# Kernel tuning notes

Measured on AMD Instinct MI355X. Metric: run time of the kernel, lower is better.

Reference implementation:

```python
import jax, jax.numpy as jnp
import numpy as np

TOPK = 2


def setup_inputs() -> dict:
    key = jax.random.key(0)
    k1, k2, k3, k4, k5 = jax.random.split(key, 5)
    D, H, E = 1024, 1408, 8
    hidden_states = jax.random.normal(k1, (2, 1024, D), dtype=jnp.float32)
    gate_w = jax.random.normal(k2, (E, D), dtype=jnp.float32) * 0.02
    w1g = jax.random.normal(k3, (E, D, H), dtype=jnp.float32) * 0.02
    w1u = jax.random.normal(k4, (E, D, H), dtype=jnp.float32) * 0.02
    w2 = jax.random.normal(k5, (E, H, D), dtype=jnp.float32) * 0.02
    return {"hidden_states": hidden_states, "gate_w": gate_w, "w1g": w1g, "w1u": w1u, "w2": w2}


def reference(hidden_states, gate_w, w1g, w1u, w2):
    # hidden_states: [B, S, D]; expert weights: w1g/w1u [E, D, H], w2 [E, H, D]
    B, S, D = hidden_states.shape
    E = gate_w.shape[0]
    x = hidden_states.reshape(-1, D)  # [T, D]
    T = x.shape[0]

    # --- MoEGate: softmax scores, top-k routing (no topk renorm) ---
    logits = x @ gate_w.T                      # [T, E]
    scores = jax.nn.softmax(logits, axis=-1)   # [T, E]
    topk_w, topk_idx = jax.lax.top_k(scores, TOPK)  # [T, K]

    # Per-token combine coefficient for each expert: coeff[t, e] = sum_k w[t,k] * (idx[t,k]==e)
    coeff = jnp.zeros((T, E), dtype=x.dtype).at[jnp.arange(T)[:, None], topk_idx].add(topk_w)

    # --- Grouped expert MLP (swiglu): identical math to permute + grouped GEMM + unpermute ---
    g = jnp.einsum('td,edh->teh', x, w1g)      # [T, E, H]
    u = jnp.einsum('td,edh->teh', x, w1u)      # [T, E, H]
    h = jax.nn.silu(g) * u                     # [T, E, H]
    y = jnp.einsum('teh,te,ehd->td', h, coeff, w2)  # [T, D]
    return y.reshape(B, S, D)
```

## Files before the change

### kernel.cpp

```cpp
#include <hip/hip_runtime.h>

#define TOK 2048
#define DDIM 1024
#define HDIM 1408
#define ENUM 8
#define NSLOT (2 * TOK)
#define UP_NB 22
#define UP_KS 32
#define DN_NB 16
#define DN_KS 44

typedef unsigned int uint;
typedef unsigned short ushort;

using bf16x8 = __attribute__((ext_vector_type(8))) __bf16;
using f32x4  = __attribute__((ext_vector_type(4))) float;

__device__ __forceinline__ float silu_f(float g) {
    return g / (1.0f + __expf(-g));
}

__device__ __forceinline__ ushort cvt_bf16(float f) {
    uint u = __float_as_uint(f);
    u += 0x7FFFu + ((u >> 16) & 1u);
    return (ushort)(u >> 16);
}

__device__ __forceinline__ void gl2lds16(const void* g, void* l) {
    __builtin_amdgcn_global_load_lds(
        (const __attribute__((address_space(1))) uint*)g,
        (__attribute__((address_space(3))) uint*)l, 16, 0, 0);
}

__global__ __launch_bounds__(64) void gate1_kernel(
    const float* __restrict__ x, const float* __restrict__ gw,
    int* __restrict__ tinfo, float* __restrict__ wslot, ushort* __restrict__ xb)
{
    const int t = blockIdx.x;
    const int lane = threadIdx.x;
    const float* xr = x + (size_t)t * DDIM;
    ushort* xbr = xb + (size_t)t * DDIM;
    float xv[16];
#pragma unroll
    for (int i = 0; i < 16; ++i) xv[i] = xr[lane + 64 * i];
#pragma unroll
    for (int i = 0; i < 16; ++i) xbr[lane + 64 * i] = cvt_bf16(xv[i]);
    float logit[ENUM];
#pragma unroll
    for (int e = 0; e < ENUM; ++e) {
        const float* gr = gw + (size_t)e * DDIM;
        float acc = 0.f;
#pragma unroll
        for (int i = 0; i < 16; ++i) acc += xv[i] * gr[lane + 64 * i];
#pragma unroll
        for (int s = 32; s > 0; s >>= 1) acc += __shfl_xor(acc, s, 64);
        logit[e] = acc;
    }
    if (lane == 0) {
        float mx = logit[0];
#pragma unroll
        for (int e = 1; e < ENUM; ++e) mx = fmaxf(mx, logit[e]);
        float p[ENUM]; float se = 0.f;
#pragma unroll
        for (int e = 0; e < ENUM; ++e) { p[e] = __expf(logit[e] - mx); se += p[e]; }
        float inv = 1.0f / se;
#pragma unroll
        for (int e = 0; e < ENUM; ++e) p[e] *= inv;
        int i0 = 0;
#pragma unroll
        for (int e = 1; e < ENUM; ++e) if (p[e] > p[i0]) i0 = e;
        int i1 = (i0 == 0) ? 1 : 0;
#pragma unroll
        for (int e = 0; e < ENUM; ++e) if (e != i0 && p[e] > p[i1]) i1 = e;
        tinfo[t] = i0 | (i1 << 4);
        wslot[(t << 1)] = p[i0];
        wslot[(t << 1) | 1] = p[i1];
    }
}

__global__ __launch_bounds__(256) void gate2_kernel(
    const int* __restrict__ tinfo, int* __restrict__ counts, int* __restrict__ toks)
{
    __shared__ int cnt[ENUM];
    const int tid = threadIdx.x;
    if (tid < ENUM) cnt[tid] = 0;
    __syncthreads();
    for (int t = tid; t < TOK; t += 256) {
        int info = tinfo[t];
        int i0 = info & 15, i1 = info >> 4;
        int p0 = atomicAdd(&cnt[i0], 1);
        toks[i0 * TOK + p0] = (t << 1);
        int p1 = atomicAdd(&cnt[i1], 1);
        toks[i1 * TOK + p1] = (t << 1) | 1;
    }
    __syncthreads();
    if (tid < ENUM) counts[tid] = cnt[tid];
}

__device__ __forceinline__ void tcast64_body(
    const float* __restrict__ src, ushort* __restrict__ dst, int N, int KS, int NB,
    int e, int ks, int nb, int tid)
{
    __shared__ float Ls[32][68];
    const float* st = src + (size_t)e * ((size_t)KS * 32) * N + (size_t)(ks * 32) * N + nb * 64;
    const int n4 = (tid & 15) * 4;
#pragma unroll
    for (int r = 0; r < 2; ++r) {
        int k = (tid >> 4) + r * 16;
        float4 v = *(const float4*)(st + (size_t)k * N + n4);
        Ls[k][n4 + 0] = v.x; Ls[k][n4 + 1] = v.y; Ls[k][n4 + 2] = v.z; Ls[k][n4 + 3] = v.w;
    }
    __syncthreads();

    ushort* dt = dst + ((((size_t)e * NB + nb) * KS) + ks) * 2048;
    const int nn = tid >> 2;
    const int kk0 = (tid & 3) * 8;
    ushort o[8];
#pragma unroll
    for (int j = 0; j < 8; ++j) o[j] = cvt_bf16(Ls[kk0 + j][nn]);
    *(uint4*)(dt + nn * 32 + kk0) = *(uint4*)o;
}

__global__ __launch_bounds__(256) void tcast_w1_kernel(
    const float* __restrict__ w1g, const float* __restrict__ w1u,
    ushort* __restrict__ BgP, ushort* __restrict__ BuP)
{
    const int z = blockIdx.z;
    const float* src = (z & 8) ? w1u : w1g;
    ushort* dst = (z & 8) ? BuP : BgP;
    tcast64_body(src, dst, HDIM, UP_KS, UP_NB, z & 7, blockIdx.x, blockIdx.y, threadIdx.x);
}

__global__ __launch_bounds__(256) void tcast_w2_kernel(
    const float* __restrict__ w2, ushort* __restrict__ W2P)
{
    tcast64_body(w2, W2P, DDIM, DN_KS, DN_NB, blockIdx.z, blockIdx.x, blockIdx.y, threadIdx.x);
}

__global__ __launch_bounds__(256, 4) void up_mfma(
    const ushort* __restrict__ xb, const ushort* __restrict__ BgP,
    const ushort* __restrict__ BuP, const int* __restrict__ counts,
    const int* __restrict__ toks, ushort* __restrict__ Hbuf)
{
    const int e = blockIdx.z;
    const int cnt = counts[e];
    const int m0 = blockIdx.y * 128;
    if (m0 >= cnt) return;
    const int nb = blockIdx.x;
    const int tid = threadIdx.x;
    const int w = tid >> 6;
    const int lane = tid & 63;
    const int q = lane >> 4;
    const int l15 = lane & 15;
    const int wr = w >> 1;
    const int wc = w & 1;

    __shared__ ushort As[2][128][32];
    __shared__ ushort Bgs[2][64][32];
    __shared__ ushort Bus[2][64][32];
    __shared__ int rowslot[128];

    if (tid < 128) rowslot[tid] = (m0 + tid < cnt) ? toks[e * TOK + m0 + tid] : -1;
    __syncthreads();

    const int srow = w * 16 + (lane >> 2);
    const int clog = (((lane & 3) + 4 - ((srow >> 1) & 3)) & 3) * 8;
    const int as0 = rowslot[srow];
    const int as1 = rowslot[srow + 64];
    const ushort* agp0 = xb + (size_t)(as0 < 0 ? 0 : (as0 >> 1)) * DDIM + clog;
    const ushort* agp1 = xb + (size_t)(as1 < 0 ? 0 : (as1 >> 1)) * DDIM + clog;
    const size_t tb = (size_t)(e * UP_NB + nb) * UP_KS * 2048;
    const ushort* bgp = BgP + tb + srow * 32 + clog;
    const ushort* bup = BuP + tb + srow * 32 + clog;

    const int coff = ((q + (l15 >> 1)) & 3) * 8;

    f32x4 accg[4][2], accu[4][2];
#pragma unroll
    for (int i = 0; i < 4; ++i)
#pragma unroll
        for (int j = 0; j < 2; ++j) { accg[i][j] = (f32x4)0.f; accu[i][j] = (f32x4)0.f; }

#define UP_PREFETCH(KSV, B)                                        \
    {                                                              \
        gl2lds16(agp0 + (KSV) * 32, &As[B][w * 16][0]);            \
        gl2lds16(agp1 + (KSV) * 32, &As[B][64 + w * 16][0]);       \
        gl2lds16(bgp + (size_t)(KSV) * 2048, &Bgs[B][w * 16][0]);  \
        gl2lds16(bup + (size_t)(KSV) * 2048, &Bus[B][w * 16][0]);  \
    }

    UP_PREFETCH(0, 0);
    __syncthreads();

    for (int ks = 0; ks < UP_KS; ++ks) {
        const int cur = ks & 1;
        const int nxt = cur ^ 1;
        if (ks + 1 < UP_KS) UP_PREFETCH(ks + 1, nxt);

        bf16x8 a[4], bg[2], bu[2];
#pragma unroll
        for (int mi = 0; mi < 4; ++mi)
            a[mi] = *(const bf16x8*)&As[cur][wr * 64 + mi * 16 + l15][coff];
#pragma unroll
        for (int ni = 0; ni < 2; ++ni) {
            bg[ni] = *(const bf16x8*)&Bgs[cur][wc * 32 + ni * 16 + l15][coff];
            bu[ni] = *(const bf16x8*)&Bus[cur][wc * 32 + ni * 16 + l15][coff];
        }
#pragma unroll
        for (int mi = 0; mi < 4; ++mi)
#pragma unroll
            for (int ni = 0; ni < 2; ++ni) {
                accg[mi][ni] = __builtin_amdgcn_mfma_f32_16x16x32_bf16(a[mi], bg[ni], accg[mi][ni], 0, 0, 0);
                accu[mi][ni] = __builtin_amdgcn_mfma_f32_16x16x32_bf16(a[mi], bu[ni], accu[mi][ni], 0, 0, 0);
            }
        __syncthreads();
    }
#undef UP_PREFETCH

#pragma unroll
    for (int mi = 0; mi < 4; ++mi) {
#pragma unroll
        for (int r = 0; r < 4; ++r) {
            int ml = wr * 64 + mi * 16 + q * 4 + r;
            int slot = rowslot[ml];
            if (slot < 0) continue;
            ushort* hrow = Hbuf + (size_t)slot * HDIM + nb * 64 + wc * 32 + l15;
#pragma unroll
            for (int ni = 0; ni < 2; ++ni)
                hrow[ni * 16] = cvt_bf16(silu_f(accg[mi][ni][r]) * accu[mi][ni][r]);
        }
    }
}

__global__ __launch_bounds__(256, 4) void down_mfma(
    const ushort* __restrict__ Hbuf, const ushort* __restrict__ W2P,
    const int* __restrict__ counts, const int* __restrict__ toks,
    float* __restrict__ Ybuf)
{
    const int e = blockIdx.z;
    const int cnt = counts[e];
    const int m0 = blockIdx.y * 128;
    if (m0 >= cnt) return;
    const int nb = blockIdx.x;
    const int tid = threadIdx.x;
    const int w = tid >> 6;
    const int lane = tid & 63;
    const int q = lane >> 4;
    const int l15 = lane & 15;
    const int wr = w >> 1;
    const int wc = w & 1;

    __shared__ ushort As[2][128][32];
    __shared__ ushort Bs[2][128][32];
    __shared__ int rowslot[128];

    if (tid < 128) rowslot[tid] = (m0 + tid < cnt) ? toks[e * TOK + m0 + tid] : -1;
    __syncthreads();

    const int srow = w * 16 + (lane >> 2);
    const int clog = (((lane & 3) + 4 - ((srow >> 1) & 3)) & 3) * 8;
    const int as0 = rowslot[srow];
    const int as1 = rowslot[srow + 64];
    const ushort* agp0 = Hbuf + (size_t)(as0 < 0 ? 0 : as0) * HDIM + clog;
    const ushort* agp1 = Hbuf + (size_t)(as1 < 0 ? 0 : as1) * HDIM + clog;
    const int nb2 = nb * 2;
    const ushort* bp0 = W2P + (size_t)(e * DN_NB + nb2) * DN_KS * 2048 + srow * 32 + clog;
    const ushort* bp1 = W2P + (size_t)(e * DN_NB + nb2 + 1) * DN_KS * 2048 + srow * 32 + clog;

    const int coff = ((q + (l15 >> 1)) & 3) * 8;

    f32x4 acc[4][4];
#pragma unroll
    for (int i = 0; i < 4; ++i)
#pragma unroll
        for (int j = 0; j < 4; ++j) acc[i][j] = (f32x4)0.f;

#define DN_PREFETCH(KSV, B)                                       \
    {                                                             \
        gl2lds16(agp0 + (KSV) * 32, &As[B][w * 16][0]);           \
        gl2lds16(agp1 + (KSV) * 32, &As[B][64 + w * 16][0]);      \
        gl2lds16(bp0 + (size_t)(KSV) * 2048, &Bs[B][w * 16][0]);  \
        gl2lds16(bp1 + (size_t)(KSV) * 2048, &Bs[B][64 + w * 16][0]); \
    }

    DN_PREFETCH(0, 0);
    __syncthreads();

    for (int ks = 0; ks < DN_KS; ++ks) {
        const int cur = ks & 1;
        const int nxt = cur ^ 1;
        if (ks + 1 < DN_KS) DN_PREFETCH(ks + 1, nxt);

        bf16x8 a[4], b[4];
#pragma unroll
        for (int mi = 0; mi < 4; ++mi)
            a[mi] = *(const bf16x8*)&As[cur][wr * 64 + mi * 16 + l15][coff];
#pragma unroll
        for (int ni = 0; ni < 4; ++ni)
            b[ni] = *(const bf16x8*)&Bs[cur][wc * 64 + ni * 16 + l15][coff];
#pragma unroll
        for (int mi = 0; mi < 4; ++mi)
#pragma unroll
            for (int ni = 0; ni < 4; ++ni)
                acc[mi][ni] = __builtin_amdgcn_mfma_f32_16x16x32_bf16(a[mi], b[ni], acc[mi][ni], 0, 0, 0);
        __syncthreads();
    }
#undef DN_PREFETCH

#pragma unroll
    for (int mi = 0; mi < 4; ++mi) {
#pragma unroll
        for (int r = 0; r < 4; ++r) {
            int ml = wr * 64 + mi * 16 + q * 4 + r;
            int slot = rowslot[ml];
            if (slot < 0) continue;
            float* yr = Ybuf + (size_t)slot * DDIM + nb * 128 + wc * 64 + l15;
#pragma unroll
            for (int ni = 0; ni < 4; ++ni)
                yr[ni * 16] = acc[mi][ni][r];
        }
    }
}

__global__ __launch_bounds__(256) void combine_kernel(
    const float* __restrict__ Ybuf, const float* __restrict__ wslot,
    float* __restrict__ y)
{
    const int t = blockIdx.x;
    const int j = threadIdx.x * 4;
    const float w0 = wslot[2 * t];
    const float w1 = wslot[2 * t + 1];
    float4 a = *(const float4*)(Ybuf + ((size_t)2 * t) * DDIM + j);
    float4 b = *(const float4*)(Ybuf + ((size_t)2 * t + 1) * DDIM + j);
    float4 o;
    o.x = w0 * a.x + w1 * b.x;
    o.y = w0 * a.y + w1 * b.y;
    o.z = w0 * a.z + w1 * b.z;
    o.w = w0 * a.w + w1 * b.w;
    *(float4*)(y + (size_t)t * DDIM + j) = o;
}

extern "C" void kernel_launch(void* const* d_in, const int* in_sizes, int n_in,
                              void* d_out, int out_size, void* d_ws, size_t ws_size,
                              hipStream_t stream) {
    const float* x   = (const float*)d_in[0];
    const float* gw  = (const float*)d_in[1];
    const float* w1g = (const float*)d_in[2];
    const float* w1u = (const float*)d_in[3];
    const float* w2  = (const float*)d_in[4];
    float* y = (float*)d_out;
    char* ws = (char*)d_ws;

    size_t off = 0;
    int*    counts = (int*)(ws + off);   off += 256;
    int*    toks   = (int*)(ws + off);   off += (size_t)ENUM * TOK * 4;
    float*  wslot  = (float*)(ws + off); off += (size_t)NSLOT * 4;
    int*    tinfo  = (int*)(ws + off);   off += (size_t)TOK * 4;
    off = (off + 255) & ~(size_t)255;
    ushort* xb     = (ushort*)(ws + off); off += (size_t)TOK * DDIM * 2;
    size_t regA = off;
    ushort* BgP  = (ushort*)(ws + regA);
    ushort* BuP  = (ushort*)(ws + regA + (size_t)ENUM * DDIM * HDIM * 2);
    float*  Ybuf = (float*)(ws + regA);
    off = regA + (size_t)2 * ENUM * DDIM * HDIM * 2;
    ushort* W2P  = (ushort*)(ws + off);  off += (size_t)ENUM * HDIM * DDIM * 2;
    ushort* Hbuf = (ushort*)(ws + off);

    gate1_kernel<<<TOK, 64, 0, stream>>>(x, gw, tinfo, wslot, xb);
    gate2_kernel<<<1, 256, 0, stream>>>(tinfo, counts, toks);

    tcast_w1_kernel<<<dim3(UP_KS, UP_NB, 16), 256, 0, stream>>>(w1g, w1u, BgP, BuP);
    tcast_w2_kernel<<<dim3(DN_KS, DN_NB, ENUM), 256, 0, stream>>>(w2, W2P);

    up_mfma<<<dim3(UP_NB, TOK / 128, ENUM), 256, 0, stream>>>(xb, BgP, BuP, counts, toks, Hbuf);
    down_mfma<<<dim3(DDIM / 128, TOK / 128, ENUM), 256, 0, stream>>>(Hbuf, W2P, counts, toks, Ybuf);
    combine_kernel<<<TOK, 256, 0, stream>>>(Ybuf, wslot, y);
}
```

Baseline: 273.5 us.

## Split down GEMM over K, fuse routing into gate, merge weight casts

The down-projection is split into two K halves, launched as extra z blocks. Each half writes a separate fp32 partial buffer, and the combine kernel sums the two. Routing is also done inside the gate kernel with global atomics after a memset, which removes the single-block gate2 kernel. The two weight-cast kernels are merged into one launch. This adds parallelism to the down GEMM and cuts launch overhead, at the cost of twice the Ybuf traffic, a larger workspace for Ybuf, and nondeterministic token order within each expert.

```diff
diff --git a/kernel.cpp b/kernel.cpp
--- a/kernel.cpp
+++ b/kernel.cpp
@@ -9,6 +9,7 @@
 #define UP_KS 32
 #define DN_NB 16
 #define DN_KS 44
+#define DN_KH 22
 
 typedef unsigned int uint;
 typedef unsigned short ushort;
@@ -34,7 +35,8 @@
 
 __global__ __launch_bounds__(64) void gate1_kernel(
     const float* __restrict__ x, const float* __restrict__ gw,
-    int* __restrict__ tinfo, float* __restrict__ wslot, ushort* __restrict__ xb)
+    int* __restrict__ counts, int* __restrict__ toks,
+    float* __restrict__ wslot, ushort* __restrict__ xb)
 {
     const int t = blockIdx.x;
     const int lane = threadIdx.x;
@@ -72,29 +74,13 @@
         int i1 = (i0 == 0) ? 1 : 0;
 #pragma unroll
         for (int e = 0; e < ENUM; ++e) if (e != i0 && p[e] > p[i1]) i1 = e;
-        tinfo[t] = i0 | (i1 << 4);
         wslot[(t << 1)] = p[i0];
         wslot[(t << 1) | 1] = p[i1];
-    }
-}
-
-__global__ __launch_bounds__(256) void gate2_kernel(
-    const int* __restrict__ tinfo, int* __restrict__ counts, int* __restrict__ toks)
-{
-    __shared__ int cnt[ENUM];
-    const int tid = threadIdx.x;
-    if (tid < ENUM) cnt[tid] = 0;
-    __syncthreads();
-    for (int t = tid; t < TOK; t += 256) {
-        int info = tinfo[t];
-        int i0 = info & 15, i1 = info >> 4;
-        int p0 = atomicAdd(&cnt[i0], 1);
+        int p0 = atomicAdd(&counts[i0], 1);
         toks[i0 * TOK + p0] = (t << 1);
-        int p1 = atomicAdd(&cnt[i1], 1);
+        int p1 = atomicAdd(&counts[i1], 1);
         toks[i1 * TOK + p1] = (t << 1) | 1;
     }
-    __syncthreads();
-    if (tid < ENUM) counts[tid] = cnt[tid];
 }
 
 __device__ __forceinline__ void tcast64_body(
@@ -121,20 +107,28 @@
     *(uint4*)(dt + nn * 32 + kk0) = *(uint4*)o;
 }
 
-__global__ __launch_bounds__(256) void tcast_w1_kernel(
+__global__ __launch_bounds__(256) void tcast_all_kernel(
     const float* __restrict__ w1g, const float* __restrict__ w1u,
-    ushort* __restrict__ BgP, ushort* __restrict__ BuP)
-{
-    const int z = blockIdx.z;
-    const float* src = (z & 8) ? w1u : w1g;
-    ushort* dst = (z & 8) ? BuP : BgP;
-    tcast64_body(src, dst, HDIM, UP_KS, UP_NB, z & 7, blockIdx.x, blockIdx.y, threadIdx.x);
-}
-
-__global__ __launch_bounds__(256) void tcast_w2_kernel(
-    const float* __restrict__ w2, ushort* __restrict__ W2P)
-{
-    tcast64_body(w2, W2P, DDIM, DN_KS, DN_NB, blockIdx.z, blockIdx.x, blockIdx.y, threadIdx.x);
+    const float* __restrict__ w2, ushort* __restrict__ BgP,
+    ushort* __restrict__ BuP, ushort* __restrict__ W2P)
+{
+    const int bid = blockIdx.x;
+    const int tid = threadIdx.x;
+    if (bid < 16 * 704) {
+        const int z = bid / 704;
+        const int rem = bid - z * 704;
+        const int nb = rem / UP_KS;
+        const int ks = rem - nb * UP_KS;
+        tcast64_body((z & 8) ? w1u : w1g, (z & 8) ? BuP : BgP,
+                     HDIM, UP_KS, UP_NB, z & 7, ks, nb, tid);
+    } else {
+        const int b2 = bid - 16 * 704;
+        const int e = b2 / 704;
+        const int rem = b2 - e * 704;
+        const int nb = rem / DN_KS;
+        const int ks = rem - nb * DN_KS;
+        tcast64_body(w2, W2P, DDIM, DN_KS, DN_NB, e, ks, nb, tid);
+    }
 }
 
 __global__ __launch_bounds__(256, 4) void up_mfma(
@@ -237,7 +231,9 @@
     const int* __restrict__ counts, const int* __restrict__ toks,
     float* __restrict__ Ybuf)
 {
-    const int e = blockIdx.z;
+    const int z = blockIdx.z;
+    const int e = z >> 1;
+    const int kh = z & 1;
     const int cnt = counts[e];
     const int m0 = blockIdx.y * 128;
     if (m0 >= cnt) return;
@@ -261,11 +257,11 @@
     const int clog = (((lane & 3) + 4 - ((srow >> 1) & 3)) & 3) * 8;
     const int as0 = rowslot[srow];
     const int as1 = rowslot[srow + 64];
-    const ushort* agp0 = Hbuf + (size_t)(as0 < 0 ? 0 : as0) * HDIM + clog;
-    const ushort* agp1 = Hbuf + (size_t)(as1 < 0 ? 0 : as1) * HDIM + clog;
+    const ushort* agp0 = Hbuf + (size_t)(as0 < 0 ? 0 : as0) * HDIM + kh * (DN_KH * 32) + clog;
+    const ushort* agp1 = Hbuf + (size_t)(as1 < 0 ? 0 : as1) * HDIM + kh * (DN_KH * 32) + clog;
     const int nb2 = nb * 2;
-    const ushort* bp0 = W2P + (size_t)(e * DN_NB + nb2) * DN_KS * 2048 + srow * 32 + clog;
-    const ushort* bp1 = W2P + (size_t)(e * DN_NB + nb2 + 1) * DN_KS * 2048 + srow * 32 + clog;
+    const ushort* bp0 = W2P + ((size_t)(e * DN_NB + nb2) * DN_KS + kh * DN_KH) * 2048 + srow * 32 + clog;
+    const ushort* bp1 = W2P + ((size_t)(e * DN_NB + nb2 + 1) * DN_KS + kh * DN_KH) * 2048 + srow * 32 + clog;
 
     const int coff = ((q + (l15 >> 1)) & 3) * 8;
 
@@ -275,21 +271,21 @@
 #pragma unroll
         for (int j = 0; j < 4; ++j) acc[i][j] = (f32x4)0.f;
 
-#define DN_PREFETCH(KSV, B)                                       \
-    {                                                             \
-        gl2lds16(agp0 + (KSV) * 32, &As[B][w * 16][0]);           \
-        gl2lds16(agp1 + (KSV) * 32, &As[B][64 + w * 16][0]);      \
-        gl2lds16(bp0 + (size_t)(KSV) * 2048, &Bs[B][w * 16][0]);  \
+#define DN_PREFETCH(KSV, B)                                           \
+    {                                                                 \
+        gl2lds16(agp0 + (KSV) * 32, &As[B][w * 16][0]);               \
+        gl2lds16(agp1 + (KSV) * 32, &As[B][64 + w * 16][0]);          \
+        gl2lds16(bp0 + (size_t)(KSV) * 2048, &Bs[B][w * 16][0]);      \
         gl2lds16(bp1 + (size_t)(KSV) * 2048, &Bs[B][64 + w * 16][0]); \
     }
 
     DN_PREFETCH(0, 0);
     __syncthreads();
 
-    for (int ks = 0; ks < DN_KS; ++ks) {
+    for (int ks = 0; ks < DN_KH; ++ks) {
         const int cur = ks & 1;
         const int nxt = cur ^ 1;
-        if (ks + 1 < DN_KS) DN_PREFETCH(ks + 1, nxt);
+        if (ks + 1 < DN_KH) DN_PREFETCH(ks + 1, nxt);
 
         bf16x8 a[4], b[4];
 #pragma unroll
@@ -307,6 +303,7 @@
     }
 #undef DN_PREFETCH
 
+    float* Yp = Ybuf + (size_t)kh * NSLOT * DDIM;
 #pragma unroll
     for (int mi = 0; mi < 4; ++mi) {
 #pragma unroll
@@ -314,7 +311,7 @@
             int ml = wr * 64 + mi * 16 + q * 4 + r;
             int slot = rowslot[ml];
             if (slot < 0) continue;
-            float* yr = Ybuf + (size_t)slot * DDIM + nb * 128 + wc * 64 + l15;
+            float* yr = Yp + (size_t)slot * DDIM + nb * 128 + wc * 64 + l15;
 #pragma unroll
             for (int ni = 0; ni < 4; ++ni)
                 yr[ni * 16] = acc[mi][ni][r];
@@ -330,13 +327,19 @@
     const int j = threadIdx.x * 4;
     const float w0 = wslot[2 * t];
     const float w1 = wslot[2 * t + 1];
-    float4 a = *(const float4*)(Ybuf + ((size_t)2 * t) * DDIM + j);
-    float4 b = *(const float4*)(Ybuf + ((size_t)2 * t + 1) * DDIM + j);
+    const float* y00 = Ybuf + ((size_t)2 * t) * DDIM + j;
+    const float* y01 = Ybuf + ((size_t)2 * t + 1) * DDIM + j;
+    const float* y10 = y00 + (size_t)NSLOT * DDIM;
+    const float* y11 = y01 + (size_t)NSLOT * DDIM;
+    float4 a0 = *(const float4*)y00;
+    float4 b0 = *(const float4*)y01;
+    float4 a1 = *(const float4*)y10;
+    float4 b1 = *(const float4*)y11;
     float4 o;
-    o.x = w0 * a.x + w1 * b.x;
-    o.y = w0 * a.y + w1 * b.y;
-    o.z = w0 * a.z + w1 * b.z;
-    o.w = w0 * a.w + w1 * b.w;
+    o.x = w0 * (a0.x + a1.x) + w1 * (b0.x + b1.x);
+    o.y = w0 * (a0.y + a1.y) + w1 * (b0.y + b1.y);
+    o.z = w0 * (a0.z + a1.z) + w1 * (b0.z + b1.z);
+    o.w = w0 * (a0.w + a1.w) + w1 * (b0.w + b1.w);
     *(float4*)(y + (size_t)t * DDIM + j) = o;
 }
 
@@ -355,7 +358,6 @@
     int*    counts = (int*)(ws + off);   off += 256;
     int*    toks   = (int*)(ws + off);   off += (size_t)ENUM * TOK * 4;
     float*  wslot  = (float*)(ws + off); off += (size_t)NSLOT * 4;
-    int*    tinfo  = (int*)(ws + off);   off += (size_t)TOK * 4;
     off = (off + 255) & ~(size_t)255;
     ushort* xb     = (ushort*)(ws + off); off += (size_t)TOK * DDIM * 2;
     size_t regA = off;
@@ -366,13 +368,11 @@
     ushort* W2P  = (ushort*)(ws + off);  off += (size_t)ENUM * HDIM * DDIM * 2;
     ushort* Hbuf = (ushort*)(ws + off);
 
-    gate1_kernel<<<TOK, 64, 0, stream>>>(x, gw, tinfo, wslot, xb);
-    gate2_kernel<<<1, 256, 0, stream>>>(tinfo, counts, toks);
-
-    tcast_w1_kernel<<<dim3(UP_KS, UP_NB, 16), 256, 0, stream>>>(w1g, w1u, BgP, BuP);
-    tcast_w2_kernel<<<dim3(DN_KS, DN_NB, ENUM), 256, 0, stream>>>(w2, W2P);
+    hipMemsetAsync(counts, 0, ENUM * sizeof(int), stream);
+    gate1_kernel<<<TOK, 64, 0, stream>>>(x, gw, counts, toks, wslot, xb);
+    tcast_all_kernel<<<16896, 256, 0, stream>>>(w1g, w1u, w2, BgP, BuP, W2P);
 
     up_mfma<<<dim3(UP_NB, TOK / 128, ENUM), 256, 0, stream>>>(xb, BgP, BuP, counts, toks, Hbuf);
-    down_mfma<<<dim3(DDIM / 128, TOK / 128, ENUM), 256, 0, stream>>>(Hbuf, W2P, counts, toks, Ybuf);
+    down_mfma<<<dim3(DDIM / 128, TOK / 128, 16), 256, 0, stream>>>(Hbuf, W2P, counts, toks, Ybuf);
     combine_kernel<<<TOK, 256, 0, stream>>>(Ybuf, wslot, y);
 }
```

New measurement: 298.0 us. 8.9% more time.
